# Performance work log

Measured on AMD Instinct MI355X. Metric: run time of the kernel, lower is better.

Reference implementation:

```python
import jax, jax.numpy as jnp
import numpy as np

EPS = 1e-06


def _conv1x1(x, W, b):
    # x: [B,C,H,W], W: [O,C], b: [O] -> [B,O,H,W]
    return jnp.einsum('oc,bchw->bohw', W, x) + b[None, :, None, None]


def _l2_norm(x):
    # normalize over channel dim (-2) per position, matching torch.norm(p=2, dim=-2)
    return x / jnp.linalg.norm(x, axis=-2, keepdims=True)


def setup_inputs() -> dict:
    key = jax.random.key(0)
    ks = jax.random.split(key, 8)
    B, C, H, W = 8, 512, 64, 64
    Cq = C // 8
    s = 0.02
    return {
        'x': jax.random.normal(ks[0], (B, C, H, W), jnp.float32),
        'Wq': jax.random.normal(ks[1], (Cq, C), jnp.float32) * s,
        'bq': jax.random.normal(ks[2], (Cq,), jnp.float32) * s,
        'Wk': jax.random.normal(ks[3], (Cq, C), jnp.float32) * s,
        'bk': jax.random.normal(ks[4], (Cq,), jnp.float32) * s,
        'Wv': jax.random.normal(ks[5], (C, C), jnp.float32) * s,
        'bv': jax.random.normal(ks[6], (C,), jnp.float32) * s,
        'gamma': jax.random.normal(ks[7], (1,), jnp.float32),
    }


def reference(x, Wq, bq, Wk, bk, Wv, bv, gamma):
    B, C, H, W = x.shape
    N = H * W
    Q = _conv1x1(x, Wq, bq).reshape(B, -1, N)   # [B,C',N]
    K = _conv1x1(x, Wk, bk).reshape(B, -1, N)   # [B,C',N]
    V = _conv1x1(x, Wv, bv).reshape(B, C, N)    # [B,C,N]

    Qn = _l2_norm(Q).transpose(0, 2, 1)         # [B,N,C']
    Kn = _l2_norm(K)                            # [B,C',N]

    # taylor denominator: 1 / (N + Q . (sum_n K + eps))
    tailor_sum = 1.0 / (N + jnp.einsum('bnc,bc->bn', Qn, Kn.sum(-1) + EPS))  # [B,N]

    value_sum = V.sum(-1)                        # [B,C]
    matrix = jnp.einsum('bmn,bcn->bmc', Kn, V)   # [B,C',C]
    matrix_sum = value_sum[:, :, None] + jnp.einsum('bnm,bmc->bcn', Qn, matrix)  # [B,C,N]

    weight_value = (matrix_sum * tailor_sum[:, None, :]).reshape(B, C, H, W)
    return gamma * weight_value
```

## Files before the change

### kernel.cpp

```cpp
#include <hip/hip_runtime.h>
#include <math.h>

#define B_   8
#define C_   512
#define CQ   64
#define N_   4096
#define EPSF 1e-6f
#define LS   40
#define LS2  72

typedef short  shortx8 __attribute__((ext_vector_type(8)));
typedef short  shortx4 __attribute__((ext_vector_type(4)));
typedef float  floatx4 __attribute__((ext_vector_type(4)));

__device__ __forceinline__ short f2bf(float f) {
    unsigned u = __builtin_bit_cast(unsigned, f);
    u += 0x7FFFu + ((u >> 16) & 1u);
    return (short)(u >> 16);
}
__device__ __forceinline__ float bf2f(short h) {
    unsigned u = ((unsigned)(unsigned short)h) << 16;
    return __builtin_bit_cast(float, u);
}
__device__ __forceinline__ shortx8 ldf8(const short* p) {
    return *(const shortx8*)p;
}

__global__ __launch_bounds__(256, 1) void k1_qk(
    const float* __restrict__ x, const float* __restrict__ Wq, const float* __restrict__ bq,
    const float* __restrict__ Wk, const float* __restrict__ bk,
    short* __restrict__ Qnt, short* __restrict__ Kn, float* __restrict__ Ksum)
{
    const int b   = blockIdx.y;
    const int n0  = blockIdx.x * 128;
    const int tid = threadIdx.x;
    const int lane = tid & 63, wid = tid >> 6;
    const int waveM = wid >> 1, waveN = wid & 1;
    const int quad = lane >> 4, ln = lane & 15;

    __shared__ short A_l[2][128][LS];
    __shared__ short B_l[2][128][LS];
    __shared__ float bias_l[128];

    if (tid < 128) bias_l[tid] = (tid < 64) ? bq[tid] : bk[tid - 64];

    const int mA  = tid >> 1, koA = (tid & 1) * 16;
    const float* Arow = (mA < 64) ? (Wq + (size_t)mA * C_) : (Wk + (size_t)(mA - 64) * C_);
    const int kB  = tid & 31, gB = tid >> 5, nbB = (tid >> 5) * 16;
    const float* xb = x + (size_t)b * C_ * N_;

    float4 aC[4], bC[4];
#pragma unroll
    for (int i = 0; i < 4; i++) aC[i] = *(const float4*)(Arow + koA + i * 4);
    {
        const float* xr = xb + (size_t)kB * N_ + n0 + nbB;
#pragma unroll
        for (int i = 0; i < 4; i++) bC[i] = *(const float4*)(xr + i * 4);
    }

    auto stage = [&](int buf, const float4* av, const float4* bv2) {
        const float* af = (const float*)av;
#pragma unroll
        for (int i = 0; i < 16; i++) A_l[buf][mA][koA + i] = f2bf(af[i]);
        const float* bf = (const float*)bv2;
#pragma unroll
        for (int i = 0; i < 16; i++) {
            int r = (i + 2 * gB) & 15;
            B_l[buf][nbB + r][kB] = f2bf(bf[r]);
        }
    };
    stage(0, aC, bC);
    __syncthreads();

    const floatx4 z4 = {0.f, 0.f, 0.f, 0.f};
    floatx4 acc[4][4];
#pragma unroll
    for (int mt = 0; mt < 4; mt++)
#pragma unroll
        for (int nt = 0; nt < 4; nt++) acc[mt][nt] = z4;

    int cur = 0;
    for (int it = 0; it < 16; ++it) {
        float4 aN[4], bN[4];
        if (it < 15) {
            const int k0 = (it + 1) * 32;
#pragma unroll
            for (int i = 0; i < 4; i++) aN[i] = *(const float4*)(Arow + k0 + koA + i * 4);
            const float* xr = xb + (size_t)(k0 + kB) * N_ + n0 + nbB;
#pragma unroll
            for (int i = 0; i < 4; i++) bN[i] = *(const float4*)(xr + i * 4);
        }
        shortx8 af4[4];
#pragma unroll
        for (int mt = 0; mt < 4; mt++)
            af4[mt] = ldf8(&A_l[cur][waveM * 64 + mt * 16 + ln][quad * 8]);
#pragma unroll
        for (int nt = 0; nt < 4; nt++) {
            shortx8 bf8 = ldf8(&B_l[cur][waveN * 64 + nt * 16 + ln][quad * 8]);
#pragma unroll
            for (int mt = 0; mt < 4; mt++)
                acc[mt][nt] = __builtin_amdgcn_mfma_f32_16x16x32_bf16(af4[mt], bf8, acc[mt][nt], 0, 0, 0);
        }
        if (it < 15) stage(cur ^ 1, aN, bN);
        __syncthreads();
        cur ^= 1;
    }

#pragma unroll
    for (int mt = 0; mt < 4; mt++)
#pragma unroll
        for (int r = 0; r < 4; r++) {
            float bias = bias_l[waveM * 64 + mt * 16 + quad * 4 + r];
#pragma unroll
            for (int nt = 0; nt < 4; nt++) acc[mt][nt][r] += bias;
        }
#pragma unroll
    for (int nt = 0; nt < 4; nt++) {
        float s = 0.f;
#pragma unroll
        for (int mt = 0; mt < 4; mt++)
#pragma unroll
            for (int r = 0; r < 4; r++) s += acc[mt][nt][r] * acc[mt][nt][r];
        s += __shfl_xor(s, 16);
        s += __shfl_xor(s, 32);
        float inv = rsqrtf(s);
#pragma unroll
        for (int mt = 0; mt < 4; mt++)
#pragma unroll
            for (int r = 0; r < 4; r++) acc[mt][nt][r] *= inv;
    }

    if (waveM == 0) {
        short* Qb = Qnt + (size_t)b * N_ * CQ;
#pragma unroll
        for (int nt = 0; nt < 4; nt++) {
            int n = n0 + waveN * 64 + nt * 16 + ln;
#pragma unroll
            for (int mt = 0; mt < 4; mt++) {
                shortx4 v;
#pragma unroll
                for (int r = 0; r < 4; r++) v[r] = f2bf(acc[mt][nt][r]);
                *(shortx4*)(Qb + (size_t)n * CQ + mt * 16 + quad * 4) = v;
            }
        }
    } else {
        short* Kb = Kn + (size_t)b * CQ * N_;
#pragma unroll
        for (int mt = 0; mt < 4; mt++)
#pragma unroll
            for (int r = 0; r < 4; r++) {
                int m = mt * 16 + quad * 4 + r;
                float s = 0.f;
#pragma unroll
                for (int nt = 0; nt < 4; nt++) {
                    int n = n0 + waveN * 64 + nt * 16 + ln;
                    float v = acc[mt][nt][r];
                    Kb[(size_t)m * N_ + n] = f2bf(v);
                    s += v;
                }
                s += __shfl_xor(s, 1); s += __shfl_xor(s, 2);
                s += __shfl_xor(s, 4); s += __shfl_xor(s, 8);
                if (ln == 0) atomicAdd(&Ksum[b * CQ + m], s);
            }
    }
}

__global__ __launch_bounds__(256, 1) void k2_kx(
    const float* __restrict__ x, const short* __restrict__ Kn,
    float* __restrict__ KX, float* __restrict__ xsum)
{
    const int jt = blockIdx.x, ks = blockIdx.y, b = blockIdx.z;
    const int j0 = jt * 128, nb0 = ks * 512;
    const int tid = threadIdx.x;
    const int lane = tid & 63, wid = tid >> 6;
    const int quad = lane >> 4, ln = lane & 15;

    __shared__ short A_l[2][64][LS];
    __shared__ short B_l[2][128][LS];

    const int mA = tid >> 2, qA = tid & 3;
    const int jB = tid >> 1, hB = tid & 1;
    const short* Kb = Kn + (size_t)b * CQ * N_;
    const float* xb = x + (size_t)b * C_ * N_;

    float xsacc = 0.f;

    shortx8 aC; float4 bC[4];
    aC = *(const shortx8*)(Kb + (size_t)mA * N_ + nb0 + qA * 8);
    {
        const float* xr = xb + (size_t)(j0 + jB) * N_ + nb0 + hB * 16;
#pragma unroll
        for (int i = 0; i < 4; i++) bC[i] = *(const float4*)(xr + i * 4);
    }
    auto stage = [&](int buf, shortx8 a, const float4* bv2) {
        *(shortx8*)&A_l[buf][mA][qA * 8] = a;
        const float* bf = (const float*)bv2;
        shortx8 t0, t1;
#pragma unroll
        for (int i = 0; i < 8; i++) {
            t0[i] = f2bf(bf[i]);     xsacc += bf[i];
            t1[i] = f2bf(bf[i + 8]); xsacc += bf[i + 8];
        }
        *(shortx8*)&B_l[buf][jB][hB * 16]     = t0;
        *(shortx8*)&B_l[buf][jB][hB * 16 + 8] = t1;
    };
    stage(0, aC, bC);
    __syncthreads();

    const floatx4 z4 = {0.f, 0.f, 0.f, 0.f};
    floatx4 acc[4][2];
#pragma unroll
    for (int mt = 0; mt < 4; mt++) { acc[mt][0] = z4; acc[mt][1] = z4; }

    int cur = 0;
    for (int it = 0; it < 16; ++it) {
        shortx8 aN; float4 bN[4];
        if (it < 15) {
            const int nn = nb0 + (it + 1) * 32;
            aN = *(const shortx8*)(Kb + (size_t)mA * N_ + nn + qA * 8);
            const float* xr = xb + (size_t)(j0 + jB) * N_ + nn + hB * 16;
#pragma unroll
            for (int i = 0; i < 4; i++) bN[i] = *(const float4*)(xr + i * 4);
        }
        shortx8 af4[4];
#pragma unroll
        for (int mt = 0; mt < 4; mt++)
            af4[mt] = ldf8(&A_l[cur][mt * 16 + ln][quad * 8]);
#pragma unroll
        for (int jt2 = 0; jt2 < 2; jt2++) {
            shortx8 bf8 = ldf8(&B_l[cur][wid * 32 + jt2 * 16 + ln][quad * 8]);
#pragma unroll
            for (int mt = 0; mt < 4; mt++)
                acc[mt][jt2] = __builtin_amdgcn_mfma_f32_16x16x32_bf16(af4[mt], bf8, acc[mt][jt2], 0, 0, 0);
        }
        if (it < 15) stage(cur ^ 1, aN, bN);
        __syncthreads();
        cur ^= 1;
    }

    xsacc += __shfl_xor(xsacc, 1);
    if (hB == 0) atomicAdd(&xsum[b * C_ + j0 + jB], xsacc);

    float* KXb = KX + (size_t)b * CQ * C_;
#pragma unroll
    for (int mt = 0; mt < 4; mt++)
#pragma unroll
        for (int jt2 = 0; jt2 < 2; jt2++)
#pragma unroll
            for (int r = 0; r < 4; r++) {
                int m = mt * 16 + quad * 4 + r;
                int j = j0 + wid * 32 + jt2 * 16 + ln;
                atomicAdd(&KXb[(size_t)m * C_ + j], acc[mt][jt2][r]);
            }
}

__global__ __launch_bounds__(256, 1) void k3_m(
    const float* __restrict__ KX, const float* __restrict__ Wv,
    const float* __restrict__ bv, const float* __restrict__ Ksum,
    const float* __restrict__ xsum,
    float* __restrict__ Mtf, float* __restrict__ vs)
{
    const int ct = blockIdx.x, jh = blockIdx.y, b = blockIdx.z;
    const int c0 = ct * 64, jb0 = jh * 128;
    const int tid = threadIdx.x;
    const int lane = tid & 63, wid = tid >> 6;
    const int quad = lane >> 4, ln = lane & 15;

    __shared__ short A_l[2][64][LS];
    __shared__ short B_l[2][64][LS];
    __shared__ float xsl[128], Ks_l[64], vsp[4][64];

    if (tid < 128) xsl[tid] = xsum[(size_t)b * C_ + jb0 + tid];
    if (tid >= 128 && tid < 192) Ks_l[tid - 128] = Ksum[b * CQ + tid - 128];

    const int rA = tid >> 2, qA = tid & 3;
    const float* Asrc = KX + ((size_t)b * CQ + rA) * C_ + jb0 + qA * 8;
    const float* Bsrc = Wv + (size_t)(c0 + rA) * C_ + jb0 + qA * 8;

    float4 aC[2], bC[2];
    aC[0] = *(const float4*)(Asrc);     aC[1] = *(const float4*)(Asrc + 4);
    bC[0] = *(const float4*)(Bsrc);     bC[1] = *(const float4*)(Bsrc + 4);

    auto stage = [&](int buf, const float4* a, const float4* bb) {
        const float* af = (const float*)a;
        const float* bf = (const float*)bb;
        shortx8 ta, tb;
#pragma unroll
        for (int i = 0; i < 8; i++) { ta[i] = f2bf(af[i]); tb[i] = f2bf(bf[i]); }
        *(shortx8*)&A_l[buf][rA][qA * 8] = ta;
        *(shortx8*)&B_l[buf][rA][qA * 8] = tb;
    };
    stage(0, aC, bC);
    __syncthreads();

    const floatx4 z4 = {0.f, 0.f, 0.f, 0.f};
    floatx4 acc[4] = {z4, z4, z4, z4};
    float vsacc = 0.f;

    int cur = 0;
    for (int it = 0; it < 4; ++it) {
        float4 aN[2], bN[2];
        if (it < 3) {
            const float* A2 = Asrc + (it + 1) * 32;
            const float* B2 = Bsrc + (it + 1) * 32;
            aN[0] = *(const float4*)(A2); aN[1] = *(const float4*)(A2 + 4);
            bN[0] = *(const float4*)(B2); bN[1] = *(const float4*)(B2 + 4);
        }
        shortx8 af4[4];
#pragma unroll
        for (int mt = 0; mt < 4; mt++)
            af4[mt] = ldf8(&A_l[cur][mt * 16 + ln][quad * 8]);
        shortx8 bf8 = ldf8(&B_l[cur][wid * 16 + ln][quad * 8]);
#pragma unroll
        for (int mt = 0; mt < 4; mt++)
            acc[mt] = __builtin_amdgcn_mfma_f32_16x16x32_bf16(af4[mt], bf8, acc[mt], 0, 0, 0);
#pragma unroll
        for (int jj = 0; jj < 8; jj++)
            vsacc += bf2f(B_l[cur][lane][wid * 8 + jj]) * xsl[it * 32 + wid * 8 + jj];
        if (it < 3) stage(cur ^ 1, aN, bN);
        __syncthreads();
        cur ^= 1;
    }

    vsp[wid][lane] = vsacc;
    __syncthreads();
    if (tid < 64)
        atomicAdd(&vs[(size_t)b * C_ + c0 + tid],
                  vsp[0][tid] + vsp[1][tid] + vsp[2][tid] + vsp[3][tid]);

    const int cl = wid * 16 + ln;
    const float bvc = bv[c0 + cl];
    float* Mb = Mtf + ((size_t)b * C_ + c0 + cl) * CQ;
#pragma unroll
    for (int mt = 0; mt < 4; mt++)
#pragma unroll
        for (int r = 0; r < 4; r++) {
            int m = mt * 16 + quad * 4 + r;
            float v = acc[mt][r];
            if (jh == 0) v += Ks_l[m] * bvc;
            atomicAdd(&Mb[m], v);
        }
}

__global__ __launch_bounds__(256, 1) void k4_out(
    const short* __restrict__ Qnt, const float* __restrict__ Mtf,
    const float* __restrict__ vs, const float* __restrict__ bv,
    const float* __restrict__ Ksum, const float* __restrict__ gamma,
    float* __restrict__ out)
{
    const int nt = blockIdx.x, ct = blockIdx.y, b = blockIdx.z;
    const int n0 = nt * 128, c0 = ct * 128;
    const int tid = threadIdx.x;
    const int lane = tid & 63, wid = tid >> 6;
    const int waveC = wid >> 1, waveN = wid & 1;
    const int quad = lane >> 4, ln = lane & 15;

    __shared__ short A_l[128][LS2];
    __shared__ short B_l[128][LS2];
    __shared__ float tsl[128], vsl[128], Ks_l[64];

    {
        int c = tid >> 1, h = tid & 1;
        const float* src = Mtf + ((size_t)b * C_ + c0 + c) * CQ + h * 32;
#pragma unroll
        for (int q = 0; q < 4; q++) {
            float4 v = *(const float4*)(src + q * 8);
            float4 w = *(const float4*)(src + q * 8 + 4);
            shortx8 t;
            t[0] = f2bf(v.x); t[1] = f2bf(v.y); t[2] = f2bf(v.z); t[3] = f2bf(v.w);
            t[4] = f2bf(w.x); t[5] = f2bf(w.y); t[6] = f2bf(w.z); t[7] = f2bf(w.w);
            *(shortx8*)&A_l[c][h * 32 + q * 8] = t;
        }
    }
    {
        int n = tid >> 1, h = tid & 1;
        const short* src = Qnt + ((size_t)b * N_ + n0 + n) * CQ + h * 32;
#pragma unroll
        for (int q = 0; q < 4; q++)
            *(shortx8*)&B_l[n][h * 32 + q * 8] = *(const shortx8*)(src + q * 8);
    }
    if (tid < 64)  Ks_l[tid] = Ksum[b * CQ + tid];
    if (tid < 128) vsl[tid]  = vs[(size_t)b * C_ + c0 + tid] + (float)N_ * bv[c0 + tid];
    __syncthreads();

    if (tid < 128) {
        const short* row = B_l[tid];
        float s = 0.f;
#pragma unroll
        for (int m = 0; m < 64; m++) s += bf2f(row[m]) * (Ks_l[m] + EPSF);
        tsl[tid] = 1.f / ((float)N_ + s);
    }
    __syncthreads();

    const floatx4 z4 = {0.f, 0.f, 0.f, 0.f};
    floatx4 acc[4][4];
#pragma unroll
    for (int i = 0; i < 4; i++)
#pragma unroll
        for (int j = 0; j < 4; j++) acc[i][j] = z4;

#pragma unroll
    for (int kc = 0; kc < 2; kc++) {
        shortx8 af4[4];
#pragma unroll
        for (int ct2 = 0; ct2 < 4; ct2++)
            af4[ct2] = ldf8(&A_l[waveC * 64 + ct2 * 16 + ln][kc * 32 + quad * 8]);
#pragma unroll
        for (int nt2 = 0; nt2 < 4; nt2++) {
            shortx8 bf8 = ldf8(&B_l[waveN * 64 + nt2 * 16 + ln][kc * 32 + quad * 8]);
#pragma unroll
            for (int ct2 = 0; ct2 < 4; ct2++)
                acc[ct2][nt2] = __builtin_amdgcn_mfma_f32_16x16x32_bf16(af4[ct2], bf8, acc[ct2][nt2], 0, 0, 0);
        }
    }

    const float g = gamma[0];
    float* ob = out + (size_t)b * C_ * N_;
#pragma unroll
    for (int ct2 = 0; ct2 < 4; ct2++)
#pragma unroll
        for (int r = 0; r < 4; r++) {
            int cl = waveC * 64 + ct2 * 16 + quad * 4 + r;
            float vc = vsl[cl];
#pragma unroll
            for (int nt2 = 0; nt2 < 4; nt2++) {
                int nl = waveN * 64 + nt2 * 16 + ln;
                ob[(size_t)(c0 + cl) * N_ + n0 + nl] = g * tsl[nl] * (vc + acc[ct2][nt2][r]);
            }
        }
}

extern "C" void kernel_launch(void* const* d_in, const int* in_sizes, int n_in,
                              void* d_out, int out_size, void* d_ws, size_t ws_size,
                              hipStream_t stream)
{
    (void)in_sizes; (void)n_in; (void)out_size; (void)ws_size;
    const float* x     = (const float*)d_in[0];
    const float* Wq    = (const float*)d_in[1];
    const float* bq    = (const float*)d_in[2];
    const float* Wk    = (const float*)d_in[3];
    const float* bk    = (const float*)d_in[4];
    const float* Wv    = (const float*)d_in[5];
    const float* bv    = (const float*)d_in[6];
    const float* gamma = (const float*)d_in[7];
    float* out = (float*)d_out;

    char* w = (char*)d_ws;
    short* Qnt = (short*)w;                 w += (size_t)B_ * N_ * CQ * 2;
    short* Kn  = (short*)w;                 w += (size_t)B_ * CQ * N_ * 2;
    float* Ksum = (float*)w;                w += (size_t)B_ * CQ * 4;
    float* xsum = (float*)w;                w += (size_t)B_ * C_ * 4;
    float* KX   = (float*)w;                w += (size_t)B_ * CQ * C_ * 4;
    float* Mtf  = (float*)w;                w += (size_t)B_ * C_ * CQ * 4;
    float* vs   = (float*)w;                w += (size_t)B_ * C_ * 4;

    size_t zbytes = (size_t)(B_ * CQ + B_ * C_ + B_ * CQ * C_ + B_ * C_ * CQ + B_ * C_) * 4;
    hipMemsetAsync(Ksum, 0, zbytes, stream);

    k1_qk <<<dim3(32, 8),    256, 0, stream>>>(x, Wq, bq, Wk, bk, Qnt, Kn, Ksum);
    k2_kx <<<dim3(4, 8, 8),  256, 0, stream>>>(x, Kn, KX, xsum);
    k3_m  <<<dim3(8, 4, 8),  256, 0, stream>>>(KX, Wv, bv, Ksum, xsum, Mtf, vs);
    k4_out<<<dim3(32, 4, 8), 256, 0, stream>>>(Qnt, Mtf, vs, bv, Ksum, gamma, out);
}
```

Baseline: 197.3 us.

## Pre-cast weights to bf16, shrink tiles for occupancy, drop atomics in M stage

Adds a small kernel that converts Wq/Wk/Wv to bf16 once per call, so the GEMM kernels load bf16 weights directly. k1 and k2 use smaller N/J tiles with coalesced x loads and launch bounds of two blocks per CU, which doubles grid size. k3 now covers the full reduction per block, so the split-K atomics on M and vs go away, and it writes M already in bf16 so k4 skips the conversion. This adds a kernel launch and extra conversion traffic, and gives up some per-block data reuse.

```diff
diff --git a/kernel.cpp b/kernel.cpp
--- a/kernel.cpp
+++ b/kernel.cpp
@@ -11,6 +11,7 @@
 
 typedef short  shortx8 __attribute__((ext_vector_type(8)));
 typedef short  shortx4 __attribute__((ext_vector_type(4)));
+typedef short  shortx2 __attribute__((ext_vector_type(2)));
 typedef float  floatx4 __attribute__((ext_vector_type(4)));
 
 __device__ __forceinline__ short f2bf(float f) {
@@ -26,82 +27,100 @@
     return *(const shortx8*)p;
 }
 
-__global__ __launch_bounds__(256, 1) void k1_qk(
-    const float* __restrict__ x, const float* __restrict__ Wq, const float* __restrict__ bq,
-    const float* __restrict__ Wk, const float* __restrict__ bk,
+__global__ __launch_bounds__(256) void pcast(
+    const float* __restrict__ Wq, const float* __restrict__ Wk,
+    const float* __restrict__ Wv, short* __restrict__ Wqk, short* __restrict__ Wvb)
+{
+    int i = (blockIdx.x * 256 + threadIdx.x) * 4;
+    float4 v; short* dst;
+    if (i < 2 * CQ * C_) {
+        const float* src = (i < CQ * C_) ? (Wq + i) : (Wk + i - CQ * C_);
+        v = *(const float4*)src;
+        dst = Wqk + i;
+    } else {
+        int j = i - 2 * CQ * C_;
+        v = *(const float4*)(Wv + j);
+        dst = Wvb + j;
+    }
+    const float* f = (const float*)&v;
+    shortx4 o = { f2bf(f[0]), f2bf(f[1]), f2bf(f[2]), f2bf(f[3]) };
+    *(shortx4*)dst = o;
+}
+
+__global__ __launch_bounds__(256, 2) void k1_qk(
+    const float* __restrict__ x, const short* __restrict__ Wqk,
+    const float* __restrict__ bq, const float* __restrict__ bk,
     short* __restrict__ Qnt, short* __restrict__ Kn, float* __restrict__ Ksum)
 {
     const int b   = blockIdx.y;
-    const int n0  = blockIdx.x * 128;
+    const int n0  = blockIdx.x * 64;
     const int tid = threadIdx.x;
     const int lane = tid & 63, wid = tid >> 6;
     const int waveM = wid >> 1, waveN = wid & 1;
     const int quad = lane >> 4, ln = lane & 15;
 
     __shared__ short A_l[2][128][LS];
-    __shared__ short B_l[2][128][LS];
+    __shared__ short B_l[2][64][LS];
     __shared__ float bias_l[128];
 
     if (tid < 128) bias_l[tid] = (tid < 64) ? bq[tid] : bk[tid - 64];
 
-    const int mA  = tid >> 1, koA = (tid & 1) * 16;
-    const float* Arow = (mA < 64) ? (Wq + (size_t)mA * C_) : (Wk + (size_t)(mA - 64) * C_);
-    const int kB  = tid & 31, gB = tid >> 5, nbB = (tid >> 5) * 16;
+    const int mA = tid >> 1, koA = (tid & 1) * 16;
+    const short* Asrc = Wqk + (size_t)mA * C_;
+    const int kp = tid >> 4, nq = tid & 15;
     const float* xb = x + (size_t)b * C_ * N_;
 
-    float4 aC[4], bC[4];
-#pragma unroll
-    for (int i = 0; i < 4; i++) aC[i] = *(const float4*)(Arow + koA + i * 4);
+    shortx8 a0 = *(const shortx8*)(Asrc + koA);
+    shortx8 a1 = *(const shortx8*)(Asrc + koA + 8);
+    float4 r0, r1;
     {
-        const float* xr = xb + (size_t)kB * N_ + n0 + nbB;
-#pragma unroll
-        for (int i = 0; i < 4; i++) bC[i] = *(const float4*)(xr + i * 4);
-    }
-
-    auto stage = [&](int buf, const float4* av, const float4* bv2) {
-        const float* af = (const float*)av;
-#pragma unroll
-        for (int i = 0; i < 16; i++) A_l[buf][mA][koA + i] = f2bf(af[i]);
-        const float* bf = (const float*)bv2;
-#pragma unroll
-        for (int i = 0; i < 16; i++) {
-            int r = (i + 2 * gB) & 15;
-            B_l[buf][nbB + r][kB] = f2bf(bf[r]);
+        const float* Bs = xb + (size_t)(kp * 2) * N_ + n0 + nq * 4;
+        r0 = *(const float4*)(Bs);
+        r1 = *(const float4*)(Bs + N_);
+    }
+
+    auto stage = [&](int buf, shortx8 s0, shortx8 s1, float4 q0, float4 q1) {
+        *(shortx8*)&A_l[buf][mA][koA]     = s0;
+        *(shortx8*)&A_l[buf][mA][koA + 8] = s1;
+        const float* f0 = (const float*)&q0;
+        const float* f1 = (const float*)&q1;
+#pragma unroll
+        for (int i = 0; i < 4; i++) {
+            shortx2 t = { f2bf(f0[i]), f2bf(f1[i]) };
+            *(shortx2*)&B_l[buf][nq * 4 + i][kp * 2] = t;
         }
     };
-    stage(0, aC, bC);
+    stage(0, a0, a1, r0, r1);
     __syncthreads();
 
     const floatx4 z4 = {0.f, 0.f, 0.f, 0.f};
-    floatx4 acc[4][4];
-#pragma unroll
-    for (int mt = 0; mt < 4; mt++)
-#pragma unroll
-        for (int nt = 0; nt < 4; nt++) acc[mt][nt] = z4;
+    floatx4 acc[4][2];
+#pragma unroll
+    for (int mt = 0; mt < 4; mt++) { acc[mt][0] = z4; acc[mt][1] = z4; }
 
     int cur = 0;
     for (int it = 0; it < 16; ++it) {
-        float4 aN[4], bN[4];
+        shortx8 na0, na1; float4 nr0, nr1;
         if (it < 15) {
             const int k0 = (it + 1) * 32;
-#pragma unroll
-            for (int i = 0; i < 4; i++) aN[i] = *(const float4*)(Arow + k0 + koA + i * 4);
-            const float* xr = xb + (size_t)(k0 + kB) * N_ + n0 + nbB;
-#pragma unroll
-            for (int i = 0; i < 4; i++) bN[i] = *(const float4*)(xr + i * 4);
-        }
-        shortx8 af4[4];
-#pragma unroll
-        for (int mt = 0; mt < 4; mt++)
-            af4[mt] = ldf8(&A_l[cur][waveM * 64 + mt * 16 + ln][quad * 8]);
-#pragma unroll
-        for (int nt = 0; nt < 4; nt++) {
-            shortx8 bf8 = ldf8(&B_l[cur][waveN * 64 + nt * 16 + ln][quad * 8]);
+            na0 = *(const shortx8*)(Asrc + k0 + koA);
+            na1 = *(const shortx8*)(Asrc + k0 + koA + 8);
+            const float* Bs = xb + (size_t)(k0 + kp * 2) * N_ + n0 + nq * 4;
+            nr0 = *(const float4*)(Bs);
+            nr1 = *(const float4*)(Bs + N_);
+        }
+        shortx8 af[4];
+#pragma unroll
+        for (int mt = 0; mt < 4; mt++)
+            af[mt] = ldf8(&A_l[cur][waveM * 64 + mt * 16 + ln][quad * 8]);
+#pragma unroll
+        for (int nt = 0; nt < 2; nt++) {
+            shortx8 bf8 = ldf8(&B_l[cur][waveN * 32 + nt * 16 + ln][quad * 8]);
 #pragma unroll
             for (int mt = 0; mt < 4; mt++)
-                acc[mt][nt] = __builtin_amdgcn_mfma_f32_16x16x32_bf16(af4[mt], bf8, acc[mt][nt], 0, 0, 0);
-        }
-        if (it < 15) stage(cur ^ 1, aN, bN);
+                acc[mt][nt] = __builtin_amdgcn_mfma_f32_16x16x32_bf16(af[mt], bf8, acc[mt][nt], 0, 0, 0);
+        }
+        if (it < 15) stage(cur ^ 1, na0, na1, nr0, nr1);
         __syncthreads();
         cur ^= 1;
     }
@@ -112,10 +131,10 @@
         for (int r = 0; r < 4; r++) {
             float bias = bias_l[waveM * 64 + mt * 16 + quad * 4 + r];
 #pragma unroll
-            for (int nt = 0; nt < 4; nt++) acc[mt][nt][r] += bias;
-        }
-#pragma unroll
-    for (int nt = 0; nt < 4; nt++) {
+            for (int nt = 0; nt < 2; nt++) acc[mt][nt][r] += bias;
+        }
+#pragma unroll
+    for (int nt = 0; nt < 2; nt++) {
         float s = 0.f;
 #pragma unroll
         for (int mt = 0; mt < 4; mt++)
@@ -133,8 +152,8 @@
     if (waveM == 0) {
         short* Qb = Qnt + (size_t)b * N_ * CQ;
 #pragma unroll
-        for (int nt = 0; nt < 4; nt++) {
-            int n = n0 + waveN * 64 + nt * 16 + ln;
+        for (int nt = 0; nt < 2; nt++) {
+            int n = n0 + waveN * 32 + nt * 16 + ln;
 #pragma unroll
             for (int mt = 0; mt < 4; mt++) {
                 shortx4 v;
@@ -152,8 +171,8 @@
                 int m = mt * 16 + quad * 4 + r;
                 float s = 0.f;
 #pragma unroll
-                for (int nt = 0; nt < 4; nt++) {
-                    int n = n0 + waveN * 64 + nt * 16 + ln;
+                for (int nt = 0; nt < 2; nt++) {
+                    int n = n0 + waveN * 32 + nt * 16 + ln;
                     float v = acc[mt][nt][r];
                     Kb[(size_t)m * N_ + n] = f2bf(v);
                     s += v;
@@ -165,188 +184,177 @@
     }
 }
 
-__global__ __launch_bounds__(256, 1) void k2_kx(
+__global__ __launch_bounds__(256, 2) void k2_kx(
     const float* __restrict__ x, const short* __restrict__ Kn,
     float* __restrict__ KX, float* __restrict__ xsum)
 {
     const int jt = blockIdx.x, ks = blockIdx.y, b = blockIdx.z;
-    const int j0 = jt * 128, nb0 = ks * 512;
+    const int j0 = jt * 64, nbase = ks * 512;
     const int tid = threadIdx.x;
     const int lane = tid & 63, wid = tid >> 6;
     const int quad = lane >> 4, ln = lane & 15;
 
     __shared__ short A_l[2][64][LS];
-    __shared__ short B_l[2][128][LS];
-
-    const int mA = tid >> 2, qA = tid & 3;
-    const int jB = tid >> 1, hB = tid & 1;
+    __shared__ short B_l[2][64][LS];
+
+    const int rA = tid >> 2, oA = (tid & 3) * 8;
     const short* Kb = Kn + (size_t)b * CQ * N_;
     const float* xb = x + (size_t)b * C_ * N_;
+    const short* As = Kb + (size_t)rA * N_ + nbase + oA;
+    const float* Bs = xb + (size_t)(j0 + rA) * N_ + nbase + oA;
 
     float xsacc = 0.f;
 
-    shortx8 aC; float4 bC[4];
-    aC = *(const shortx8*)(Kb + (size_t)mA * N_ + nb0 + qA * 8);
-    {
-        const float* xr = xb + (size_t)(j0 + jB) * N_ + nb0 + hB * 16;
-#pragma unroll
-        for (int i = 0; i < 4; i++) bC[i] = *(const float4*)(xr + i * 4);
-    }
-    auto stage = [&](int buf, shortx8 a, const float4* bv2) {
-        *(shortx8*)&A_l[buf][mA][qA * 8] = a;
-        const float* bf = (const float*)bv2;
-        shortx8 t0, t1;
-#pragma unroll
-        for (int i = 0; i < 8; i++) {
-            t0[i] = f2bf(bf[i]);     xsacc += bf[i];
-            t1[i] = f2bf(bf[i + 8]); xsacc += bf[i + 8];
-        }
-        *(shortx8*)&B_l[buf][jB][hB * 16]     = t0;
-        *(shortx8*)&B_l[buf][jB][hB * 16 + 8] = t1;
+    shortx8 aC = *(const shortx8*)As;
+    float4 b0 = *(const float4*)(Bs);
+    float4 b1 = *(const float4*)(Bs + 4);
+
+    auto stage = [&](int buf, shortx8 a, float4 q0, float4 q1) {
+        *(shortx8*)&A_l[buf][rA][oA] = a;
+        const float* f0 = (const float*)&q0;
+        const float* f1 = (const float*)&q1;
+        shortx8 t;
+#pragma unroll
+        for (int i = 0; i < 4; i++) {
+            t[i]     = f2bf(f0[i]); xsacc += f0[i];
+            t[i + 4] = f2bf(f1[i]); xsacc += f1[i];
+        }
+        *(shortx8*)&B_l[buf][rA][oA] = t;
     };
-    stage(0, aC, bC);
+    stage(0, aC, b0, b1);
     __syncthreads();
 
     const floatx4 z4 = {0.f, 0.f, 0.f, 0.f};
-    floatx4 acc[4][2];
-#pragma unroll
-    for (int mt = 0; mt < 4; mt++) { acc[mt][0] = z4; acc[mt][1] = z4; }
+    floatx4 acc[4] = {z4, z4, z4, z4};
 
     int cur = 0;
     for (int it = 0; it < 16; ++it) {
-        shortx8 aN; float4 bN[4];
+        shortx8 aN; float4 n0v, n1v;
         if (it < 15) {
-            const int nn = nb0 + (it + 1) * 32;
-            aN = *(const shortx8*)(Kb + (size_t)mA * N_ + nn + qA * 8);
-            const float* xr = xb + (size_t)(j0 + jB) * N_ + nn + hB * 16;
-#pragma unroll
-            for (int i = 0; i < 4; i++) bN[i] = *(const float4*)(xr + i * 4);
-        }
-        shortx8 af4[4];
-#pragma unroll
-        for (int mt = 0; mt < 4; mt++)
-            af4[mt] = ldf8(&A_l[cur][mt * 16 + ln][quad * 8]);
-#pragma unroll
-        for (int jt2 = 0; jt2 < 2; jt2++) {
-            shortx8 bf8 = ldf8(&B_l[cur][wid * 32 + jt2 * 16 + ln][quad * 8]);
-#pragma unroll
-            for (int mt = 0; mt < 4; mt++)
-                acc[mt][jt2] = __builtin_amdgcn_mfma_f32_16x16x32_bf16(af4[mt], bf8, acc[mt][jt2], 0, 0, 0);
-        }
-        if (it < 15) stage(cur ^ 1, aN, bN);
+            const int off = (it + 1) * 32;
+            aN  = *(const shortx8*)(As + off);
+            n0v = *(const float4*)(Bs + off);
+            n1v = *(const float4*)(Bs + off + 4);
+        }
+        shortx8 af[4];
+#pragma unroll
+        for (int mt = 0; mt < 4; mt++)
+            af[mt] = ldf8(&A_l[cur][mt * 16 + ln][quad * 8]);
+        shortx8 bf8 = ldf8(&B_l[cur][wid * 16 + ln][quad * 8]);
+#pragma unroll
+        for (int mt = 0; mt < 4; mt++)
+            acc[mt] = __builtin_amdgcn_mfma_f32_16x16x32_bf16(af[mt], bf8, acc[mt], 0, 0, 0);
+        if (it < 15) stage(cur ^ 1, aN, n0v, n1v);
         __syncthreads();
         cur ^= 1;
     }
 
     xsacc += __shfl_xor(xsacc, 1);
-    if (hB == 0) atomicAdd(&xsum[b * C_ + j0 + jB], xsacc);
+    xsacc += __shfl_xor(xsacc, 2);
+    if ((tid & 3) == 0) atomicAdd(&xsum[b * C_ + j0 + rA], xsacc);
 
     float* KXb = KX + (size_t)b * CQ * C_;
 #pragma unroll
     for (int mt = 0; mt < 4; mt++)
 #pragma unroll
-        for (int jt2 = 0; jt2 < 2; jt2++)
-#pragma unroll
-            for (int r = 0; r < 4; r++) {
-                int m = mt * 16 + quad * 4 + r;
-                int j = j0 + wid * 32 + jt2 * 16 + ln;
-                atomicAdd(&KXb[(size_t)m * C_ + j], acc[mt][jt2][r]);
-            }
-}
-
-__global__ __launch_bounds__(256, 1) void k3_m(
-    const float* __restrict__ KX, const float* __restrict__ Wv,
+        for (int r = 0; r < 4; r++) {
+            int m = mt * 16 + quad * 4 + r;
+            atomicAdd(&KXb[(size_t)m * C_ + j0 + wid * 16 + ln], acc[mt][r]);
+        }
+}
+
+__global__ __launch_bounds__(256, 2) void k3_m(
+    const float* __restrict__ KX, const short* __restrict__ Wvb,
     const float* __restrict__ bv, const float* __restrict__ Ksum,
     const float* __restrict__ xsum,
-    float* __restrict__ Mtf, float* __restrict__ vs)
-{
-    const int ct = blockIdx.x, jh = blockIdx.y, b = blockIdx.z;
-    const int c0 = ct * 64, jb0 = jh * 128;
+    short* __restrict__ Mt, float* __restrict__ vs)
+{
+    const int ct = blockIdx.x, b = blockIdx.y;
+    const int c0 = ct * 64;
     const int tid = threadIdx.x;
     const int lane = tid & 63, wid = tid >> 6;
     const int quad = lane >> 4, ln = lane & 15;
 
     __shared__ short A_l[2][64][LS];
     __shared__ short B_l[2][64][LS];
-    __shared__ float xsl[128], Ks_l[64], vsp[4][64];
-
-    if (tid < 128) xsl[tid] = xsum[(size_t)b * C_ + jb0 + tid];
-    if (tid >= 128 && tid < 192) Ks_l[tid - 128] = Ksum[b * CQ + tid - 128];
-
-    const int rA = tid >> 2, qA = tid & 3;
-    const float* Asrc = KX + ((size_t)b * CQ + rA) * C_ + jb0 + qA * 8;
-    const float* Bsrc = Wv + (size_t)(c0 + rA) * C_ + jb0 + qA * 8;
-
-    float4 aC[2], bC[2];
-    aC[0] = *(const float4*)(Asrc);     aC[1] = *(const float4*)(Asrc + 4);
-    bC[0] = *(const float4*)(Bsrc);     bC[1] = *(const float4*)(Bsrc + 4);
-
-    auto stage = [&](int buf, const float4* a, const float4* bb) {
-        const float* af = (const float*)a;
-        const float* bf = (const float*)bb;
-        shortx8 ta, tb;
-#pragma unroll
-        for (int i = 0; i < 8; i++) { ta[i] = f2bf(af[i]); tb[i] = f2bf(bf[i]); }
-        *(shortx8*)&A_l[buf][rA][qA * 8] = ta;
-        *(shortx8*)&B_l[buf][rA][qA * 8] = tb;
+    __shared__ float xsl[C_], Ksl[64], bvl[64], vsp[4][64];
+
+    xsl[tid] = xsum[(size_t)b * C_ + tid];
+    xsl[tid + 256] = xsum[(size_t)b * C_ + tid + 256];
+    if (tid < 64) { Ksl[tid] = Ksum[b * CQ + tid]; bvl[tid] = bv[c0 + tid]; }
+
+    const int rA = tid >> 2, oA = (tid & 3) * 8;
+    const short* As = Wvb + (size_t)(c0 + rA) * C_ + oA;
+    const float* Bs = KX + ((size_t)b * CQ + rA) * C_ + oA;
+
+    shortx8 aC = *(const shortx8*)As;
+    float4 b0 = *(const float4*)(Bs);
+    float4 b1 = *(const float4*)(Bs + 4);
+
+    auto stage = [&](int buf, shortx8 a, float4 q0, float4 q1) {
+        *(shortx8*)&A_l[buf][rA][oA] = a;
+        const float* f0 = (const float*)&q0;
+        const float* f1 = (const float*)&q1;
+        shortx8 t;
+#pragma unroll
+        for (int i = 0; i < 4; i++) { t[i] = f2bf(f0[i]); t[i + 4] = f2bf(f1[i]); }
+        *(shortx8*)&B_l[buf][rA][oA] = t;
     };
-    stage(0, aC, bC);
+    stage(0, aC, b0, b1);
     __syncthreads();
 
     const floatx4 z4 = {0.f, 0.f, 0.f, 0.f};
     floatx4 acc[4] = {z4, z4, z4, z4};
     float vsacc = 0.f;
+    const int cv = tid & 63;
 
     int cur = 0;
-    for (int it = 0; it < 4; ++it) {
-        float4 aN[2], bN[2];
-        if (it < 3) {
-            const float* A2 = Asrc + (it + 1) * 32;
-            const float* B2 = Bsrc + (it + 1) * 32;
-            aN[0] = *(const float4*)(A2); aN[1] = *(const float4*)(A2 + 4);
-            bN[0] = *(const float4*)(B2); bN[1] = *(const float4*)(B2 + 4);
-        }
-        shortx8 af4[4];
-#pragma unroll
-        for (int mt = 0; mt < 4; mt++)
-            af4[mt] = ldf8(&A_l[cur][mt * 16 + ln][quad * 8]);
+    for (int it = 0; it < 16; ++it) {
+        shortx8 aN; float4 n0v, n1v;
+        if (it < 15) {
+            const int off = (it + 1) * 32;
+            aN  = *(const shortx8*)(As + off);
+            n0v = *(const float4*)(Bs + off);
+            n1v = *(const float4*)(Bs + off + 4);
+        }
+        shortx8 af[4];
+#pragma unroll
+        for (int ct2 = 0; ct2 < 4; ct2++)
+            af[ct2] = ldf8(&A_l[cur][ct2 * 16 + ln][quad * 8]);
         shortx8 bf8 = ldf8(&B_l[cur][wid * 16 + ln][quad * 8]);
 #pragma unroll
-        for (int mt = 0; mt < 4; mt++)
-            acc[mt] = __builtin_amdgcn_mfma_f32_16x16x32_bf16(af4[mt], bf8, acc[mt], 0, 0, 0);
+        for (int ct2 = 0; ct2 < 4; ct2++)
+            acc[ct2] = __builtin_amdgcn_mfma_f32_16x16x32_bf16(af[ct2], bf8, acc[ct2], 0, 0, 0);
 #pragma unroll
         for (int jj = 0; jj < 8; jj++)
-            vsacc += bf2f(B_l[cur][lane][wid * 8 + jj]) * xsl[it * 32 + wid * 8 + jj];
-        if (it < 3) stage(cur ^ 1, aN, bN);
+            vsacc += bf2f(A_l[cur][cv][wid * 8 + jj]) * xsl[it * 32 + wid * 8 + jj];
+        if (it < 15) stage(cur ^ 1, aN, n0v, n1v);
         __syncthreads();
         cur ^= 1;
     }
 
-    vsp[wid][lane] = vsacc;
+    vsp[wid][cv] = vsacc;
     __syncthreads();
     if (tid < 64)
-        atomicAdd(&vs[(size_t)b * C_ + c0 + tid],
-                  vsp[0][tid] + vsp[1][tid] + vsp[2][tid] + vsp[3][tid]);
-
-    const int cl = wid * 16 + ln;
-    const float bvc = bv[c0 + cl];
-    float* Mb = Mtf + ((size_t)b * C_ + c0 + cl) * CQ;
-#pragma unroll
-    for (int mt = 0; mt < 4; mt++)
+        vs[(size_t)b * C_ + c0 + tid] =
+            vsp[0][tid] + vsp[1][tid] + vsp[2][tid] + vsp[3][tid] + (float)N_ * bvl[tid];
+
+    const int m = wid * 16 + ln;
+    const float ksm = Ksl[m];
+    short* Mb = Mt + (size_t)b * C_ * CQ;
+#pragma unroll
+    for (int ct2 = 0; ct2 < 4; ct2++)
 #pragma unroll
         for (int r = 0; r < 4; r++) {
-            int m = mt * 16 + quad * 4 + r;
-            float v = acc[mt][r];
-            if (jh == 0) v += Ks_l[m] * bvc;
-            atomicAdd(&Mb[m], v);
-        }
-}
-
-__global__ __launch_bounds__(256, 1) void k4_out(
-    const short* __restrict__ Qnt, const float* __restrict__ Mtf,
-    const float* __restrict__ vs, const float* __restrict__ bv,
-    const float* __restrict__ Ksum, const float* __restrict__ gamma,
-    float* __restrict__ out)
+            int c = ct2 * 16 + quad * 4 + r;
+            Mb[(size_t)(c0 + c) * CQ + m] = f2bf(acc[ct2][r] + ksm * bvl[c]);
+        }
+}
+
+__global__ __launch_bounds__(256, 2) void k4_out(
+    const short* __restrict__ Qnt, const short* __restrict__ Mt,
+    const float* __restrict__ vs, const float* __restrict__ Ksum,
+    const float* __restrict__ gamma, float* __restrict__ out)
 {
     const int nt = blockIdx.x, ct = blockIdx.y, b = blockIdx.z;
     const int n0 = nt * 128, c0 = ct * 128;
@@ -361,16 +369,10 @@
 
     {
         int c = tid >> 1, h = tid & 1;
-        const float* src = Mtf + ((size_t)b * C_ + c0 + c) * CQ + h * 32;
-#pragma unroll
-        for (int q = 0; q < 4; q++) {
-            float4 v = *(const float4*)(src + q * 8);
-            float4 w = *(const float4*)(src + q * 8 + 4);
-            shortx8 t;
-            t[0] = f2bf(v.x); t[1] = f2bf(v.y); t[2] = f2bf(v.z); t[3] = f2bf(v.w);
-            t[4] = f2bf(w.x); t[5] = f2bf(w.y); t[6] = f2bf(w.z); t[7] = f2bf(w.w);
-            *(shortx8*)&A_l[c][h * 32 + q * 8] = t;
-        }
+        const short* src = Mt + ((size_t)b * C_ + c0 + c) * CQ + h * 32;
+#pragma unroll
+        for (int q = 0; q < 4; q++)
+            *(shortx8*)&A_l[c][h * 32 + q * 8] = *(const shortx8*)(src + q * 8);
     }
     {
         int n = tid >> 1, h = tid & 1;
@@ -380,7 +382,7 @@
             *(shortx8*)&B_l[n][h * 32 + q * 8] = *(const shortx8*)(src + q * 8);
     }
     if (tid < 64)  Ks_l[tid] = Ksum[b * CQ + tid];
-    if (tid < 128) vsl[tid]  = vs[(size_t)b * C_ + c0 + tid] + (float)N_ * bv[c0 + tid];
+    if (tid < 128) vsl[tid]  = vs[(size_t)b * C_ + c0 + tid];
     __syncthreads();
 
     if (tid < 128) {
@@ -401,16 +403,16 @@
 
 #pragma unroll
     for (int kc = 0; kc < 2; kc++) {
-        shortx8 af4[4];
+        shortx8 af[4];
 #pragma unroll
         for (int ct2 = 0; ct2 < 4; ct2++)
-            af4[ct2] = ldf8(&A_l[waveC * 64 + ct2 * 16 + ln][kc * 32 + quad * 8]);
+            af[ct2] = ldf8(&A_l[waveC * 64 + ct2 * 16 + ln][kc * 32 + quad * 8]);
 #pragma unroll
         for (int nt2 = 0; nt2 < 4; nt2++) {
             shortx8 bf8 = ldf8(&B_l[waveN * 64 + nt2 * 16 + ln][kc * 32 + quad * 8]);
 #pragma unroll
             for (int ct2 = 0; ct2 < 4; ct2++)
-                acc[ct2][nt2] = __builtin_amdgcn_mfma_f32_16x16x32_bf16(af4[ct2], bf8, acc[ct2][nt2], 0, 0, 0);
+                acc[ct2][nt2] = __builtin_amdgcn_mfma_f32_16x16x32_bf16(af[ct2], bf8, acc[ct2][nt2], 0, 0, 0);
         }
     }
 
@@ -445,20 +447,22 @@
     const float* gamma = (const float*)d_in[7];
     float* out = (float*)d_out;
 
-    char* w = (char*)d_ws;
-    short* Qnt = (short*)w;                 w += (size_t)B_ * N_ * CQ * 2;
-    short* Kn  = (short*)w;                 w += (size_t)B_ * CQ * N_ * 2;
-    float* Ksum = (float*)w;                w += (size_t)B_ * CQ * 4;
-    float* xsum = (float*)w;                w += (size_t)B_ * C_ * 4;
-    float* KX   = (float*)w;                w += (size_t)B_ * CQ * C_ * 4;
-    float* Mtf  = (float*)w;                w += (size_t)B_ * C_ * CQ * 4;
-    float* vs   = (float*)w;                w += (size_t)B_ * C_ * 4;
-
-    size_t zbytes = (size_t)(B_ * CQ + B_ * C_ + B_ * CQ * C_ + B_ * C_ * CQ + B_ * C_) * 4;
+    short* Qnt = (short*)d_ws;
+    short* Kn  = Qnt + (size_t)B_ * N_ * CQ;
+    float* Ksum = (float*)(Kn + (size_t)B_ * CQ * N_);
+    float* xsum = Ksum + B_ * CQ;
+    float* KX   = xsum + B_ * C_;
+    short* Mt   = (short*)(KX + (size_t)B_ * CQ * C_);
+    float* vs   = (float*)(Mt + (size_t)B_ * C_ * CQ);
+    short* Wqk  = (short*)(vs + B_ * C_);
+    short* Wvb  = Wqk + 2 * CQ * C_;
+
+    size_t zbytes = (size_t)(B_ * CQ + B_ * C_ + B_ * CQ * C_) * 4;
     hipMemsetAsync(Ksum, 0, zbytes, stream);
 
-    k1_qk <<<dim3(32, 8),    256, 0, stream>>>(x, Wq, bq, Wk, bk, Qnt, Kn, Ksum);
-    k2_kx <<<dim3(4, 8, 8),  256, 0, stream>>>(x, Kn, KX, xsum);
-    k3_m  <<<dim3(8, 4, 8),  256, 0, stream>>>(KX, Wv, bv, Ksum, xsum, Mtf, vs);
-    k4_out<<<dim3(32, 4, 8), 256, 0, stream>>>(Qnt, Mtf, vs, bv, Ksum, gamma, out);
-}
+    pcast <<<dim3(320),      256, 0, stream>>>(Wq, Wk, Wv, Wqk, Wvb);
+    k1_qk <<<dim3(64, 8),    256, 0, stream>>>(x, Wqk, bq, bk, Qnt, Kn, Ksum);
+    k2_kx <<<dim3(8, 8, 8),  256, 0, stream>>>(x, Kn, KX, xsum);
+    k3_m  <<<dim3(8, 8),     256, 0, stream>>>(KX, Wvb, bv, Ksum, xsum, Mt, vs);
+    k4_out<<<dim3(32, 4, 8), 256, 0, stream>>>(Qnt, Mt, vs, Ksum, gamma, out);
+}
```

Result: faster. 185.4 us (-6.0%).
